# Kernel tuning notes

Hardware: AMD Instinct MI355X
Metric: run time of the kernel (lower is better)

Reference implementation:

```python
import jax, jax.numpy as jnp
import numpy as np

B, SQ, SK = 2, 2048, 2048
D_MODEL, N_HEADS = 1024, 16
D_HEAD = D_MODEL // N_HEADS
LN_EPS = 1e-5


def _ln(x, w, b):
    # per-head LayerNorm over last dim (d_head)
    mu = jnp.mean(x, axis=-1, keepdims=True)
    var = jnp.mean(jnp.square(x - mu), axis=-1, keepdims=True)
    return (x - mu) * jax.lax.rsqrt(var + LN_EPS) * w + b


def setup_inputs() -> dict:
    key = jax.random.key(0)
    ks = jax.random.split(key, 8)
    sd = 1.0 / np.sqrt(D_MODEL)
    so = 1.0 / np.sqrt(D_HEAD)
    return {
        "x_q": jax.random.normal(ks[0], (B, SQ, D_MODEL), jnp.float32),
        "x_kv": jax.random.normal(ks[1], (B, SK, D_MODEL), jnp.float32),
        "mask": jnp.tril(jnp.ones((SQ, SK), dtype=bool)),  # causal
        "W_Q": jax.random.normal(ks[2], (N_HEADS, D_MODEL, D_HEAD), jnp.float32) * sd,
        "W_K": jax.random.normal(ks[3], (N_HEADS, D_MODEL, D_HEAD), jnp.float32) * sd,
        "W_V": jax.random.normal(ks[4], (N_HEADS, D_MODEL, D_HEAD), jnp.float32) * sd,
        "W_O": jax.random.normal(ks[5], (N_HEADS, D_HEAD, D_MODEL), jnp.float32) * so,
        "b_Q": jnp.zeros((N_HEADS, D_HEAD), jnp.float32),
        "b_K": jnp.zeros((N_HEADS, D_HEAD), jnp.float32),
        "b_V": jnp.zeros((N_HEADS, D_HEAD), jnp.float32),
        "b_O": jnp.zeros((D_MODEL,), jnp.float32),
        "ln1_w": jnp.ones((D_HEAD,), jnp.float32),
        "ln1_b": jnp.zeros((D_HEAD,), jnp.float32),
        "ln2_w": jnp.ones((D_HEAD,), jnp.float32),
        "ln2_b": jnp.zeros((D_HEAD,), jnp.float32),
    }


def reference(x_q, x_kv, mask, W_Q, W_K, W_V, W_O, b_Q, b_K, b_V, b_O,
              ln1_w, ln1_b, ln2_w, ln2_b):
    # QKV projections: b s d, n d h -> b s n h
    q = jnp.einsum('bsd,ndh->bsnh', x_q, W_Q) + b_Q
    k = jnp.einsum('bsd,ndh->bsnh', x_kv, W_K) + b_K
    v = jnp.einsum('bsd,ndh->bsnh', x_kv, W_V) + b_V
    # QK-norm (ln_first=False, rope=None -> just apply LN after projections)
    q = _ln(q, ln1_w, ln1_b)
    k = _ln(k, ln2_w, ln2_b)
    # NOTE: no 1/sqrt(d_head) scaling, matching the original module
    att = jnp.einsum('bqnh,bknh->bnqk', q, k)
    att = jnp.where(mask, att, -jnp.inf)
    probas = jax.nn.softmax(att, axis=-1)
    z = jnp.einsum('bnqk,bknh->bqnh', probas, v)
    out = jnp.einsum('bqnh,nhd->bqd', z, W_O) + b_O
    return (out, k, v)
```

## Files before the change

kernel.cpp:

```cpp
#include <hip/hip_runtime.h>
#include <hip/hip_bf16.h>

#define B_   2
#define SQ_  2048
#define DM_  1024
#define NH_  16
#define DH_  64

typedef __attribute__((ext_vector_type(8))) short          bf16x8;
typedef __attribute__((ext_vector_type(8))) unsigned short u16x8;
typedef __attribute__((ext_vector_type(4))) float          f32x4;

__device__ __forceinline__ unsigned short f2bf(float f) {
    union { __hip_bfloat16 h; unsigned short u; } c;
    c.h = __float2bfloat16(f);
    return c.u;
}
__device__ __forceinline__ float gsum16(float v) {
    v += __shfl_xor(v, 1);
    v += __shfl_xor(v, 2);
    v += __shfl_xor(v, 4);
    v += __shfl_xor(v, 8);
    return v;
}

__device__ __forceinline__ void gll16(const unsigned short* g, unsigned short* l) {
    __builtin_amdgcn_global_load_lds(
        (const __attribute__((address_space(1))) unsigned int*)g,
        (__attribute__((address_space(3))) unsigned int*)l,
        16, 0, 0);
}

__global__ __launch_bounds__(256) void prep_all(
    const float* __restrict__ W_Q, const float* __restrict__ W_K,
    const float* __restrict__ W_V, const float* __restrict__ W_O,
    const float* __restrict__ x_q, const float* __restrict__ x_kv,
    unsigned short* __restrict__ WTq, unsigned short* __restrict__ WTkv,
    unsigned short* __restrict__ WTo,
    unsigned short* __restrict__ xqbf, unsigned short* __restrict__ xkvbf)
{
    const int bid = blockIdx.x, tid = threadIdx.x;
    if (bid >= 1024) {
        const int cid = bid - 1024;
        const float* src = (cid < 256) ? x_q : x_kv;
        unsigned short* dst = (cid < 256) ? xqbf : xkvbf;
        const size_t base = (size_t)(cid & 255) * 16384 + tid * 4;
#pragma unroll
        for (int i = 0; i < 16; ++i) {
            const float4 v = *(const float4*)(src + base + i * 1024);
            ushort4 o;
            o.x = f2bf(v.x); o.y = f2bf(v.y); o.z = f2bf(v.z); o.w = f2bf(v.w);
            *(ushort4*)(dst + base + i * 1024) = o;
        }
        return;
    }
    __shared__ float t[64][65];
    const float* src; unsigned short* dst; int R, C, r0, c0;
    if (bid < 768) {
        const int which = bid >> 8, rem = bid & 255;
        const int rblk = rem & 15, zz = rem >> 4;
        src = (which == 0) ? W_Q : (which == 1) ? W_K : W_V;
        dst = (which == 0) ? WTq : (which == 1) ? WTkv : (WTkv + (1u << 20));
        src += (size_t)65536 * zz;
        dst += (size_t)65536 * zz;
        R = 1024; C = 64; r0 = rblk * 64; c0 = 0;
    } else {
        const int rem = bid - 768;
        src = W_O; dst = WTo; R = 1024; C = 1024;
        r0 = (rem & 15) * 64; c0 = (rem >> 4) * 64;
    }
    const int lr = tid >> 6, lc = tid & 63;
#pragma unroll
    for (int i = 0; i < 16; ++i)
        t[lr + i * 4][lc] = src[(size_t)(r0 + lr + i * 4) * C + c0 + lc];
    __syncthreads();
#pragma unroll
    for (int i = 0; i < 16; ++i)
        dst[(size_t)(c0 + lr + i * 4) * R + r0 + lc] = f2bf(t[lc][lr + i * 4]);
}

template <int TN, int MODE>
__device__ __forceinline__ void gemm_body(
    unsigned short (*__restrict__ As)[64], unsigned short (*__restrict__ Bs)[64],
    int bx, int by, const unsigned short* __restrict__ Abf,
    const unsigned short* __restrict__ WT,
    const float* __restrict__ biasK, const float* __restrict__ biasV,
    const float* __restrict__ lnw, const float* __restrict__ lnb,
    float* __restrict__ Cf, float* __restrict__ Cf2,
    unsigned short* __restrict__ Cb, unsigned short* __restrict__ CbT, int tid)
{
    constexpr int MI = (TN == 128) ? 4 : 2;
    constexpr int BP = TN / 64;

    const int m0 = by * 128;
    const int c0 = bx * TN;

    const int wid = tid >> 6, lane = tid & 63;
    const int wm = (TN == 128) ? (wid >> 1) * 64 : wid * 32;
    const int wn = (TN == 128) ? (wid & 1) * 64 : 0;
    const int l15 = lane & 15, qd = lane >> 4;

    const int srow = tid >> 3, scol = (tid & 7) * 8;
    const unsigned short* Ag = Abf + (size_t)(m0 + srow) * 1024 + scol;
    const unsigned short* Bg = WT  + (size_t)(c0 + srow) * 1024 + scol;
    unsigned short* Al = &As[srow][scol];
    unsigned short* Bl = &Bs[srow][scol];

    const f32x4 zero4 = {0.f, 0.f, 0.f, 0.f};
    f32x4 acc[MI][4];
#pragma unroll
    for (int mi = 0; mi < MI; ++mi)
#pragma unroll
        for (int ni = 0; ni < 4; ++ni) acc[mi][ni] = zero4;

    for (int kb = 0; kb < 16; ++kb) {
        const size_t kof = (size_t)kb * 64;
        __syncthreads();
#pragma unroll
        for (int j = 0; j < 4; ++j)
            gll16(Ag + (size_t)j * 32 * 1024 + kof, Al + j * 32 * 64);
#pragma unroll
        for (int j = 0; j < 2 * BP; ++j)
            gll16(Bg + (size_t)j * 32 * 1024 + kof, Bl + j * 32 * 64);
        __syncthreads();
#pragma unroll
        for (int ks = 0; ks < 2; ++ks) {
            bf16x8 af[MI], bfr[4];
#pragma unroll
            for (int mi = 0; mi < MI; ++mi)
                af[mi] = *(const bf16x8*)&As[wm + mi * 16 + l15][ks * 32 + qd * 8];
#pragma unroll
            for (int ni = 0; ni < 4; ++ni)
                bfr[ni] = *(const bf16x8*)&Bs[wn + ni * 16 + l15][ks * 32 + qd * 8];
#pragma unroll
            for (int mi = 0; mi < MI; ++mi)
#pragma unroll
                for (int ni = 0; ni < 4; ++ni)
                    acc[mi][ni] = __builtin_amdgcn_mfma_f32_16x16x32_bf16(
                        af[mi], bfr[ni], acc[mi][ni], 0, 0, 0);
        }
    }

    const float* bias = (MODE == 1 && c0 >= 1024) ? biasV : biasK;
    float bv[4];
#pragma unroll
    for (int ni = 0; ni < 4; ++ni) bv[ni] = bias[(c0 + wn + ni * 16 + l15) & 1023];
#pragma unroll
    for (int mi = 0; mi < MI; ++mi)
#pragma unroll
        for (int ni = 0; ni < 4; ++ni)
#pragma unroll
            for (int r = 0; r < 4; ++r) acc[mi][ni][r] += bv[ni];

    if constexpr (MODE != 2) {
        const bool doLN = (MODE == 0) || (c0 < 1024);
        if (doLN) {
            float w4[4], lb4[4];
#pragma unroll
            for (int ni = 0; ni < 4; ++ni) {
                w4[ni]  = lnw[ni * 16 + l15];
                lb4[ni] = lnb[ni * 16 + l15];
            }
#pragma unroll
            for (int mi = 0; mi < MI; ++mi)
#pragma unroll
                for (int r = 0; r < 4; ++r) {
                    float s1 = acc[mi][0][r] + acc[mi][1][r] + acc[mi][2][r] + acc[mi][3][r];
                    const float mu = gsum16(s1) * (1.0f / 64.0f);
                    float s2 = acc[mi][0][r] * acc[mi][0][r] + acc[mi][1][r] * acc[mi][1][r]
                             + acc[mi][2][r] * acc[mi][2][r] + acc[mi][3][r] * acc[mi][3][r];
                    const float var = gsum16(s2) * (1.0f / 64.0f) - mu * mu;
                    const float rstd = rsqrtf(var + 1e-5f);
#pragma unroll
                    for (int ni = 0; ni < 4; ++ni)
                        acc[mi][ni][r] = (acc[mi][ni][r] - mu) * rstd * w4[ni] + lb4[ni];
                }
        }
    }

    if constexpr (MODE == 0) {
#pragma unroll
        for (int mi = 0; mi < MI; ++mi)
#pragma unroll
            for (int r = 0; r < 4; ++r) {
                const size_t grow = m0 + wm + mi * 16 + qd * 4 + r;
#pragma unroll
                for (int ni = 0; ni < 4; ++ni)
                    Cb[grow * 1024 + c0 + wn + ni * 16 + l15] = f2bf(acc[mi][ni][r]);
            }
    } else if constexpr (MODE == 2) {
#pragma unroll
        for (int mi = 0; mi < MI; ++mi)
#pragma unroll
            for (int r = 0; r < 4; ++r) {
                const size_t grow = m0 + wm + mi * 16 + qd * 4 + r;
#pragma unroll
                for (int ni = 0; ni < 4; ++ni)
                    Cf[grow * 1024 + c0 + wn + ni * 16 + l15] = acc[mi][ni][r];
            }
    } else {
        if (c0 < 1024) {
#pragma unroll
            for (int mi = 0; mi < MI; ++mi)
#pragma unroll
                for (int r = 0; r < 4; ++r) {
                    const size_t grow = m0 + wm + mi * 16 + qd * 4 + r;
#pragma unroll
                    for (int ni = 0; ni < 4; ++ni) {
                        const int gcol = c0 + wn + ni * 16 + l15;
                        Cf[grow * 1024 + gcol] = acc[mi][ni][r];
                        Cb[grow * 1024 + gcol] = f2bf(acc[mi][ni][r]);
                    }
                }
        } else {
#pragma unroll
            for (int mi = 0; mi < MI; ++mi) {
                const int growb = m0 + wm + mi * 16 + qd * 4;
                const int bb_ = growb >> 11, ss = growb & 2047;
#pragma unroll
                for (int ni = 0; ni < 4; ++ni) {
                    const int gv = c0 - 1024 + wn + ni * 16 + l15;
                    const int hh = gv >> 6, dd = gv & 63;
#pragma unroll
                    for (int r = 0; r < 4; ++r)
                        Cf2[(size_t)(growb + r) * 1024 + gv] = acc[mi][ni][r];
                    ushort4 w;
                    w.x = f2bf(acc[mi][ni][0]); w.y = f2bf(acc[mi][ni][1]);
                    w.z = f2bf(acc[mi][ni][2]); w.w = f2bf(acc[mi][ni][3]);
                    *(ushort4*)&CbT[(((size_t)bb_ * NH_ + hh) * DH_ + dd) * SQ_ + ss] = w;
                }
            }
        }
    }
}

__global__ __launch_bounds__(256) void qkv_fused(
    const unsigned short* __restrict__ xqbf, const unsigned short* __restrict__ xkvbf,
    const unsigned short* __restrict__ WTq, const unsigned short* __restrict__ WTkv,
    const float* __restrict__ b_Q, const float* __restrict__ b_K,
    const float* __restrict__ b_V,
    const float* __restrict__ ln1w, const float* __restrict__ ln1b,
    const float* __restrict__ ln2w, const float* __restrict__ ln2b,
    float* __restrict__ kout, float* __restrict__ vout,
    unsigned short* __restrict__ qz, unsigned short* __restrict__ kbf,
    unsigned short* __restrict__ vbfT)
{
    __shared__ __align__(16) unsigned short As[128][64];
    __shared__ __align__(16) unsigned short Bs[128][64];
    const int bid = blockIdx.x, tid = threadIdx.x;
    if (bid < 512) {
        gemm_body<128, 1>(As, Bs, bid & 15, bid >> 4, xkvbf, WTkv, b_K, b_V,
                          ln2w, ln2b, kout, vout, kbf, vbfT, tid);
    } else {
        const int b2 = bid - 512;
        gemm_body<128, 0>(As, Bs, b2 & 7, b2 >> 3, xqbf, WTq, b_Q, nullptr,
                          ln1w, ln1b, nullptr, nullptr, qz, nullptr, tid);
    }
}

__global__ __launch_bounds__(256) void o_gemm(
    const unsigned short* __restrict__ zbf, const unsigned short* __restrict__ WTo,
    const float* __restrict__ b_O, float* __restrict__ out)
{
    __shared__ __align__(16) unsigned short As[128][64];
    __shared__ __align__(16) unsigned short Bs[64][64];
    gemm_body<64, 2>(As, Bs, blockIdx.x, blockIdx.y, zbf, WTo, b_O, nullptr,
                     nullptr, nullptr, out, nullptr, nullptr, nullptr, threadIdx.x);
}

__global__ __launch_bounds__(256) void attn_mfma(
    unsigned short* __restrict__ qz, const unsigned short* __restrict__ kbf,
    const unsigned short* __restrict__ vbfT)
{
    __shared__ __align__(16) unsigned short Ks[64][72];
    __shared__ __align__(16) unsigned short VsT[64][72];
    __shared__ __align__(16) unsigned short Ps[64][72];

    const int tid = threadIdx.x;
    const int h = blockIdx.y, b = blockIdx.z;
    const int wid = tid >> 6, lane = tid & 63;
    const int l15 = lane & 15, qd = lane >> 4;
    const int srow = tid >> 2, scol = (tid & 3) * 16;

    const size_t kbase = (size_t)b * SQ_ * DM_ + (size_t)h * DH_;
    const size_t vbase = ((size_t)b * NH_ + h) * DH_ * (size_t)SQ_;
    const f32x4 zero4 = {0.f, 0.f, 0.f, 0.f};

    const int qt = 31 - (int)blockIdx.x;

    bf16x8 qf[2];
    {
        const unsigned short* qp =
            qz + kbase + (size_t)(qt * 64 + wid * 16 + l15) * DM_ + qd * 8;
        qf[0] = *(const bf16x8*)(qp);
        qf[1] = *(const bf16x8*)(qp + 32);
    }

    f32x4 z[4];
#pragma unroll
    for (int ni = 0; ni < 4; ++ni) z[ni] = zero4;
    float m_i = -3.0e38f, l_i = 0.f;

    u16x8 kr0, kr1, vr0, vr1;
    {
        const unsigned short* ks = kbf + kbase + (size_t)srow * DM_ + scol;
        kr0 = *(const u16x8*)(ks);
        kr1 = *(const u16x8*)(ks + 8);
        const unsigned short* vs = vbfT + vbase + (size_t)srow * SQ_ + scol;
        vr0 = *(const u16x8*)(vs);
        vr1 = *(const u16x8*)(vs + 8);
    }

    for (int kt = 0; kt <= qt; ++kt) {
        __syncthreads();
        *(u16x8*)&Ks[srow][scol + 0]  = kr0;
        *(u16x8*)&Ks[srow][scol + 8]  = kr1;
        *(u16x8*)&VsT[srow][scol + 0] = vr0;
        *(u16x8*)&VsT[srow][scol + 8] = vr1;
        __syncthreads();
        if (kt < qt) {
            const unsigned short* ks =
                kbf + kbase + (size_t)((kt + 1) * 64 + srow) * DM_ + scol;
            kr0 = *(const u16x8*)(ks);
            kr1 = *(const u16x8*)(ks + 8);
            const unsigned short* vs =
                vbfT + vbase + (size_t)srow * SQ_ + (kt + 1) * 64 + scol;
            vr0 = *(const u16x8*)(vs);
            vr1 = *(const u16x8*)(vs + 8);
        }

        f32x4 s[4];
#pragma unroll
        for (int mi = 0; mi < 4; ++mi) s[mi] = zero4;
#pragma unroll
        for (int ks2 = 0; ks2 < 2; ++ks2)
#pragma unroll
            for (int mi = 0; mi < 4; ++mi) {
                const bf16x8 af = *(const bf16x8*)&Ks[mi * 16 + l15][ks2 * 32 + qd * 8];
                s[mi] = __builtin_amdgcn_mfma_f32_16x16x32_bf16(af, qf[ks2], s[mi], 0, 0, 0);
            }

        if (kt == qt) {
#pragma unroll
            for (int mi = 0; mi < 4; ++mi)
#pragma unroll
                for (int r = 0; r < 4; ++r)
                    if (mi * 16 + qd * 4 + r > wid * 16 + l15) s[mi][r] = -3.0e38f;
        }

        float mloc = -3.0e38f;
#pragma unroll
        for (int mi = 0; mi < 4; ++mi)
#pragma unroll
            for (int r = 0; r < 4; ++r) mloc = fmaxf(mloc, s[mi][r]);
        mloc = fmaxf(mloc, __shfl_xor(mloc, 16));
        mloc = fmaxf(mloc, __shfl_xor(mloc, 32));
        const float mn = fmaxf(m_i, mloc);
        const float alpha = __expf(m_i - mn);
        float rs = 0.f;
#pragma unroll
        for (int mi = 0; mi < 4; ++mi)
#pragma unroll
            for (int r = 0; r < 4; ++r) {
                const float e = __expf(s[mi][r] - mn);
                s[mi][r] = e;
                rs += e;
            }
        rs += __shfl_xor(rs, 16);
        rs += __shfl_xor(rs, 32);
        l_i = l_i * alpha + rs;
        m_i = mn;

#pragma unroll
        for (int mi = 0; mi < 4; ++mi) {
            ushort4 w;
            w.x = f2bf(s[mi][0]); w.y = f2bf(s[mi][1]);
            w.z = f2bf(s[mi][2]); w.w = f2bf(s[mi][3]);
            *(ushort4*)&Ps[wid * 16 + l15][mi * 16 + qd * 4] = w;
        }

#pragma unroll
        for (int r = 0; r < 4; ++r) {
            const float ar = __shfl(alpha, qd * 4 + r);
#pragma unroll
            for (int ni = 0; ni < 4; ++ni) z[ni][r] *= ar;
        }

#pragma unroll
        for (int ks2 = 0; ks2 < 2; ++ks2) {
            const bf16x8 ap = *(const bf16x8*)&Ps[wid * 16 + l15][ks2 * 32 + qd * 8];
#pragma unroll
            for (int ni = 0; ni < 4; ++ni) {
                const bf16x8 bv = *(const bf16x8*)&VsT[ni * 16 + l15][ks2 * 32 + qd * 8];
                z[ni] = __builtin_amdgcn_mfma_f32_16x16x32_bf16(ap, bv, z[ni], 0, 0, 0);
            }
        }
    }

    const float linv = 1.0f / l_i;
#pragma unroll
    for (int r = 0; r < 4; ++r) {
        const float lr_ = __shfl(linv, qd * 4 + r);
        const size_t row = (size_t)qt * 64 + wid * 16 + qd * 4 + r;
#pragma unroll
        for (int ni = 0; ni < 4; ++ni)
            qz[kbase + row * DM_ + ni * 16 + l15] = f2bf(z[ni][r] * lr_);
    }
}

extern "C" void kernel_launch(void* const* d_in, const int* in_sizes, int n_in,
                              void* d_out, int out_size, void* d_ws, size_t ws_size,
                              hipStream_t stream)
{
    const float* x_q  = (const float*)d_in[0];
    const float* x_kv = (const float*)d_in[1];
    const float* W_Q  = (const float*)d_in[3];
    const float* W_K  = (const float*)d_in[4];
    const float* W_V  = (const float*)d_in[5];
    const float* W_O  = (const float*)d_in[6];
    const float* b_Q  = (const float*)d_in[7];
    const float* b_K  = (const float*)d_in[8];
    const float* b_V  = (const float*)d_in[9];
    const float* b_O  = (const float*)d_in[10];
    const float* ln1w = (const float*)d_in[11];
    const float* ln1b = (const float*)d_in[12];
    const float* ln2w = (const float*)d_in[13];
    const float* ln2b = (const float*)d_in[14];

    const size_t NTOK = (size_t)B_ * SQ_;
    float* out  = (float*)d_out;
    float* kout = out + NTOK * DM_;
    float* vout = kout + NTOK * DM_;

    unsigned short* xqbf  = (unsigned short*)out;
    unsigned short* xkvbf = xqbf + (1u << 22);

    unsigned short* wsu  = (unsigned short*)d_ws;
    unsigned short* WTq  = wsu;
    unsigned short* WTkv = WTq + (1u << 20);
    unsigned short* WTo  = WTkv + (2u << 20);
    unsigned short* qz   = WTo + (1u << 20);
    unsigned short* kbf  = qz + (1u << 22);
    unsigned short* vbfT = kbf + (1u << 22);

    prep_all<<<1536, 256, 0, stream>>>(W_Q, W_K, W_V, W_O, x_q, x_kv,
                                       WTq, WTkv, WTo, xqbf, xkvbf);

    qkv_fused<<<768, 256, 0, stream>>>(xqbf, xkvbf, WTq, WTkv, b_Q, b_K, b_V,
                                       ln1w, ln1b, ln2w, ln2b,
                                       kout, vout, qz, kbf, vbfT);

    attn_mfma<<<dim3(32, NH_, B_), 256, 0, stream>>>(qz, kbf, vbfT);

    o_gemm<<<dim3(16, 32), 256, 0, stream>>>(qz, WTo, b_O, out);
}
```

Measured before the change: 281.5 us.

## Pair causal query tiles per block and double-buffer K/V tiles in LDS

Each attention block now processes two query tiles (qt and 31-qt) sequentially, balancing causal work, and the grid is halved. K/V tiles are double-buffered in shared memory so the next tile's store happens after compute with a single barrier per iteration. This reduces load imbalance and barrier count, at the cost of fewer resident blocks and more LDS per block.

```diff
diff --git a/kernel.cpp b/kernel.cpp
--- a/kernel.cpp
+++ b/kernel.cpp
@@ -272,8 +272,8 @@
     unsigned short* __restrict__ qz, const unsigned short* __restrict__ kbf,
     const unsigned short* __restrict__ vbfT)
 {
-    __shared__ __align__(16) unsigned short Ks[64][72];
-    __shared__ __align__(16) unsigned short VsT[64][72];
+    __shared__ __align__(16) unsigned short Ks[2][64][72];
+    __shared__ __align__(16) unsigned short VsT[2][64][72];
     __shared__ __align__(16) unsigned short Ps[64][72];
 
     const int tid = threadIdx.x;
@@ -286,125 +286,138 @@
     const size_t vbase = ((size_t)b * NH_ + h) * DH_ * (size_t)SQ_;
     const f32x4 zero4 = {0.f, 0.f, 0.f, 0.f};
 
-    const int qt = 31 - (int)blockIdx.x;
-
-    bf16x8 qf[2];
-    {
-        const unsigned short* qp =
-            qz + kbase + (size_t)(qt * 64 + wid * 16 + l15) * DM_ + qd * 8;
-        qf[0] = *(const bf16x8*)(qp);
-        qf[1] = *(const bf16x8*)(qp + 32);
-    }
-
-    f32x4 z[4];
-#pragma unroll
-    for (int ni = 0; ni < 4; ++ni) z[ni] = zero4;
-    float m_i = -3.0e38f, l_i = 0.f;
-
-    u16x8 kr0, kr1, vr0, vr1;
-    {
-        const unsigned short* ks = kbf + kbase + (size_t)srow * DM_ + scol;
-        kr0 = *(const u16x8*)(ks);
-        kr1 = *(const u16x8*)(ks + 8);
-        const unsigned short* vs = vbfT + vbase + (size_t)srow * SQ_ + scol;
-        vr0 = *(const u16x8*)(vs);
-        vr1 = *(const u16x8*)(vs + 8);
-    }
-
-    for (int kt = 0; kt <= qt; ++kt) {
+    for (int pass = 0; pass < 2; ++pass) {
+        const int qt = pass ? blockIdx.x : 31 - blockIdx.x;
+
+        bf16x8 qf[2];
+        {
+            const unsigned short* qp =
+                qz + kbase + (size_t)(qt * 64 + wid * 16 + l15) * DM_ + qd * 8;
+            qf[0] = *(const bf16x8*)(qp);
+            qf[1] = *(const bf16x8*)(qp + 32);
+        }
+
+        f32x4 z[4];
+#pragma unroll
+        for (int ni = 0; ni < 4; ++ni) z[ni] = zero4;
+        float m_i = -3.0e38f, l_i = 0.f;
+
+        {
+            const unsigned short* ks = kbf + kbase + (size_t)srow * DM_ + scol;
+            const u16x8 a0 = *(const u16x8*)(ks);
+            const u16x8 a1 = *(const u16x8*)(ks + 8);
+            const unsigned short* vs = vbfT + vbase + (size_t)srow * SQ_ + scol;
+            const u16x8 b0 = *(const u16x8*)(vs);
+            const u16x8 b1 = *(const u16x8*)(vs + 8);
+            *(u16x8*)&Ks[0][srow][scol + 0]  = a0;
+            *(u16x8*)&Ks[0][srow][scol + 8]  = a1;
+            *(u16x8*)&VsT[0][srow][scol + 0] = b0;
+            *(u16x8*)&VsT[0][srow][scol + 8] = b1;
+        }
         __syncthreads();
-        *(u16x8*)&Ks[srow][scol + 0]  = kr0;
-        *(u16x8*)&Ks[srow][scol + 8]  = kr1;
-        *(u16x8*)&VsT[srow][scol + 0] = vr0;
-        *(u16x8*)&VsT[srow][scol + 8] = vr1;
-        __syncthreads();
-        if (kt < qt) {
-            const unsigned short* ks =
-                kbf + kbase + (size_t)((kt + 1) * 64 + srow) * DM_ + scol;
-            kr0 = *(const u16x8*)(ks);
-            kr1 = *(const u16x8*)(ks + 8);
-            const unsigned short* vs =
-                vbfT + vbase + (size_t)srow * SQ_ + (kt + 1) * 64 + scol;
-            vr0 = *(const u16x8*)(vs);
-            vr1 = *(const u16x8*)(vs + 8);
-        }
-
-        f32x4 s[4];
-#pragma unroll
-        for (int mi = 0; mi < 4; ++mi) s[mi] = zero4;
-#pragma unroll
-        for (int ks2 = 0; ks2 < 2; ++ks2)
+
+        for (int kt = 0; kt <= qt; ++kt) {
+            const int cur = kt & 1;
+
+            u16x8 kr0, kr1, vr0, vr1;
+            if (kt < qt) {
+                const unsigned short* ks =
+                    kbf + kbase + (size_t)((kt + 1) * 64 + srow) * DM_ + scol;
+                kr0 = *(const u16x8*)(ks);
+                kr1 = *(const u16x8*)(ks + 8);
+                const unsigned short* vs =
+                    vbfT + vbase + (size_t)srow * SQ_ + (kt + 1) * 64 + scol;
+                vr0 = *(const u16x8*)(vs);
+                vr1 = *(const u16x8*)(vs + 8);
+            }
+
+            f32x4 s[4];
+#pragma unroll
+            for (int mi = 0; mi < 4; ++mi) s[mi] = zero4;
+#pragma unroll
+            for (int ks2 = 0; ks2 < 2; ++ks2)
+#pragma unroll
+                for (int mi = 0; mi < 4; ++mi) {
+                    const bf16x8 af =
+                        *(const bf16x8*)&Ks[cur][mi * 16 + l15][ks2 * 32 + qd * 8];
+                    s[mi] = __builtin_amdgcn_mfma_f32_16x16x32_bf16(af, qf[ks2], s[mi], 0, 0, 0);
+                }
+
+            if (kt == qt) {
+#pragma unroll
+                for (int mi = 0; mi < 4; ++mi)
+#pragma unroll
+                    for (int r = 0; r < 4; ++r)
+                        if (mi * 16 + qd * 4 + r > wid * 16 + l15) s[mi][r] = -3.0e38f;
+            }
+
+            float mloc = -3.0e38f;
+#pragma unroll
+            for (int mi = 0; mi < 4; ++mi)
+#pragma unroll
+                for (int r = 0; r < 4; ++r) mloc = fmaxf(mloc, s[mi][r]);
+            mloc = fmaxf(mloc, __shfl_xor(mloc, 16));
+            mloc = fmaxf(mloc, __shfl_xor(mloc, 32));
+            const float mn = fmaxf(m_i, mloc);
+            const float alpha = __expf(m_i - mn);
+            float rs = 0.f;
+#pragma unroll
+            for (int mi = 0; mi < 4; ++mi)
+#pragma unroll
+                for (int r = 0; r < 4; ++r) {
+                    const float e = __expf(s[mi][r] - mn);
+                    s[mi][r] = e;
+                    rs += e;
+                }
+            rs += __shfl_xor(rs, 16);
+            rs += __shfl_xor(rs, 32);
+            l_i = l_i * alpha + rs;
+            m_i = mn;
+
 #pragma unroll
             for (int mi = 0; mi < 4; ++mi) {
-                const bf16x8 af = *(const bf16x8*)&Ks[mi * 16 + l15][ks2 * 32 + qd * 8];
-                s[mi] = __builtin_amdgcn_mfma_f32_16x16x32_bf16(af, qf[ks2], s[mi], 0, 0, 0);
-            }
-
-        if (kt == qt) {
-#pragma unroll
-            for (int mi = 0; mi < 4; ++mi)
-#pragma unroll
-                for (int r = 0; r < 4; ++r)
-                    if (mi * 16 + qd * 4 + r > wid * 16 + l15) s[mi][r] = -3.0e38f;
-        }
-
-        float mloc = -3.0e38f;
-#pragma unroll
-        for (int mi = 0; mi < 4; ++mi)
-#pragma unroll
-            for (int r = 0; r < 4; ++r) mloc = fmaxf(mloc, s[mi][r]);
-        mloc = fmaxf(mloc, __shfl_xor(mloc, 16));
-        mloc = fmaxf(mloc, __shfl_xor(mloc, 32));
-        const float mn = fmaxf(m_i, mloc);
-        const float alpha = __expf(m_i - mn);
-        float rs = 0.f;
-#pragma unroll
-        for (int mi = 0; mi < 4; ++mi)
+                ushort4 w;
+                w.x = f2bf(s[mi][0]); w.y = f2bf(s[mi][1]);
+                w.z = f2bf(s[mi][2]); w.w = f2bf(s[mi][3]);
+                *(ushort4*)&Ps[wid * 16 + l15][mi * 16 + qd * 4] = w;
+            }
+
 #pragma unroll
             for (int r = 0; r < 4; ++r) {
-                const float e = __expf(s[mi][r] - mn);
-                s[mi][r] = e;
-                rs += e;
-            }
-        rs += __shfl_xor(rs, 16);
-        rs += __shfl_xor(rs, 32);
-        l_i = l_i * alpha + rs;
-        m_i = mn;
-
-#pragma unroll
-        for (int mi = 0; mi < 4; ++mi) {
-            ushort4 w;
-            w.x = f2bf(s[mi][0]); w.y = f2bf(s[mi][1]);
-            w.z = f2bf(s[mi][2]); w.w = f2bf(s[mi][3]);
-            *(ushort4*)&Ps[wid * 16 + l15][mi * 16 + qd * 4] = w;
-        }
-
+                const float ar = __shfl(alpha, qd * 4 + r);
+#pragma unroll
+                for (int ni = 0; ni < 4; ++ni) z[ni][r] *= ar;
+            }
+
+#pragma unroll
+            for (int ks2 = 0; ks2 < 2; ++ks2) {
+                const bf16x8 ap = *(const bf16x8*)&Ps[wid * 16 + l15][ks2 * 32 + qd * 8];
+#pragma unroll
+                for (int ni = 0; ni < 4; ++ni) {
+                    const bf16x8 bv =
+                        *(const bf16x8*)&VsT[cur][ni * 16 + l15][ks2 * 32 + qd * 8];
+                    z[ni] = __builtin_amdgcn_mfma_f32_16x16x32_bf16(ap, bv, z[ni], 0, 0, 0);
+                }
+            }
+
+            if (kt < qt) {
+                *(u16x8*)&Ks[cur ^ 1][srow][scol + 0]  = kr0;
+                *(u16x8*)&Ks[cur ^ 1][srow][scol + 8]  = kr1;
+                *(u16x8*)&VsT[cur ^ 1][srow][scol + 0] = vr0;
+                *(u16x8*)&VsT[cur ^ 1][srow][scol + 8] = vr1;
+            }
+            __syncthreads();
+        }
+
+        const float linv = 1.0f / l_i;
 #pragma unroll
         for (int r = 0; r < 4; ++r) {
-            const float ar = __shfl(alpha, qd * 4 + r);
-#pragma unroll
-            for (int ni = 0; ni < 4; ++ni) z[ni][r] *= ar;
-        }
-
-#pragma unroll
-        for (int ks2 = 0; ks2 < 2; ++ks2) {
-            const bf16x8 ap = *(const bf16x8*)&Ps[wid * 16 + l15][ks2 * 32 + qd * 8];
-#pragma unroll
-            for (int ni = 0; ni < 4; ++ni) {
-                const bf16x8 bv = *(const bf16x8*)&VsT[ni * 16 + l15][ks2 * 32 + qd * 8];
-                z[ni] = __builtin_amdgcn_mfma_f32_16x16x32_bf16(ap, bv, z[ni], 0, 0, 0);
-            }
-        }
-    }
-
-    const float linv = 1.0f / l_i;
-#pragma unroll
-    for (int r = 0; r < 4; ++r) {
-        const float lr_ = __shfl(linv, qd * 4 + r);
-        const size_t row = (size_t)qt * 64 + wid * 16 + qd * 4 + r;
-#pragma unroll
-        for (int ni = 0; ni < 4; ++ni)
-            qz[kbase + row * DM_ + ni * 16 + l15] = f2bf(z[ni][r] * lr_);
+            const float lr_ = __shfl(linv, qd * 4 + r);
+            const size_t row = (size_t)qt * 64 + wid * 16 + qd * 4 + r;
+#pragma unroll
+            for (int ni = 0; ni < 4; ++ni)
+                qz[kbase + row * DM_ + ni * 16 + l15] = f2bf(z[ni][r] * lr_);
+        }
     }
 }
 
@@ -450,7 +463,7 @@
                                        ln1w, ln1b, ln2w, ln2b,
                                        kout, vout, qz, kbf, vbfT);
 
-    attn_mfma<<<dim3(32, NH_, B_), 256, 0, stream>>>(qz, kbf, vbfT);
+    attn_mfma<<<dim3(16, NH_, B_), 256, 0, stream>>>(qz, kbf, vbfT);
 
     o_gemm<<<dim3(16, 32), 256, 0, stream>>>(qz, WTo, b_O, out);
 }
```

Result: faster. 254.6 us (-9.6%).
